# Optimization experiments

Measured on AMD Instinct MI355X. Metric: run time of the kernel, lower is better.

The kernel has to match this reference:

```python
import jax, jax.numpy as jnp
import numpy as np

N, E, B, T = 50000, 800000, 256, 50
IN_DIM, H, C1, C2, Q_DIM, LH = 128, 4, 32, 128, 32, 128
EPS = 1e-5


def setup_inputs() -> dict:
    key = jax.random.key(0)
    ks = jax.random.split(key, 24)
    g = 0.05
    inp = {
        'x': jax.random.normal(ks[0], (N, IN_DIM), jnp.float32),
        'edge_index': jax.random.randint(ks[1], (2, E), 0, N, jnp.int32),
        'batch': jnp.sort(jax.random.randint(ks[2], (N,), 0, B, jnp.int32)),
        'quant': jax.random.normal(ks[3], (B, T, Q_DIM), jnp.float32),
        # GATConv(128 -> 32, heads=4, concat)
        'gat_W': jax.random.normal(ks[4], (IN_DIM, H * C1), jnp.float32) * g,
        'gat_att_src': jax.random.normal(ks[5], (H, C1), jnp.float32) * g,
        'gat_att_dst': jax.random.normal(ks[6], (H, C1), jnp.float32) * g,
        'gat_b': jnp.zeros((H * C1,), jnp.float32),
        # BN1 over 128 channels (eval mode)
        'bn1_gamma': jnp.ones((H * C1,), jnp.float32),
        'bn1_beta': jnp.zeros((H * C1,), jnp.float32),
        'bn1_mean': jax.random.normal(ks[7], (H * C1,), jnp.float32) * 0.01,
        'bn1_var': jnp.ones((H * C1,), jnp.float32),
        # GCNConv(128 -> 128)
        'gcn_W': jax.random.normal(ks[8], (H * C1, C2), jnp.float32) * g,
        'gcn_b': jnp.zeros((C2,), jnp.float32),
        'bn2_gamma': jnp.ones((C2,), jnp.float32),
        'bn2_beta': jnp.zeros((C2,), jnp.float32),
        'bn2_mean': jax.random.normal(ks[9], (C2,), jnp.float32) * 0.01,
        'bn2_var': jnp.ones((C2,), jnp.float32),
        # GlobalAttention gate: Linear(C2 -> 1)
        'gate_W': jax.random.normal(ks[10], (1, C2), jnp.float32) * g,
        'gate_b': jnp.zeros((1,), jnp.float32),
        # LSTM(Q_DIM -> LH), torch gate order i,f,g,o
        'lstm_Wih': jax.random.normal(ks[11], (4 * LH, Q_DIM), jnp.float32) * g,
        'lstm_Whh': jax.random.normal(ks[12], (4 * LH, LH), jnp.float32) * g,
        'lstm_bih': jnp.zeros((4 * LH,), jnp.float32),
        'lstm_bhh': jnp.zeros((4 * LH,), jnp.float32),
        # final Linear(C2+LH -> 1)
        'fc_W': jax.random.normal(ks[13], (1, C2 + LH), jnp.float32) * g,
        'fc_b': jnp.zeros((1,), jnp.float32),
    }
    return inp


def _segment_softmax(e, seg, num_segments):
    m = jax.ops.segment_max(e, seg, num_segments=num_segments)
    ex = jnp.exp(e - m[seg])
    s = jax.ops.segment_sum(ex, seg, num_segments=num_segments)
    return ex / (s[seg] + 1e-16)


def _bn_eval(x, gamma, beta, mean, var):
    return gamma * (x - mean) * jax.lax.rsqrt(var + EPS) + beta


def _forward(x, edge_index, batch, quant,
             gat_W, gat_att_src, gat_att_dst, gat_b,
             bn1_gamma, bn1_beta, bn1_mean, bn1_var,
             gcn_W, gcn_b, bn2_gamma, bn2_beta, bn2_mean, bn2_var,
             gate_W, gate_b,
             lstm_Wih, lstm_Whh, lstm_bih, lstm_bhh,
             fc_W, fc_b):
    n = x.shape[0]
    loops = jnp.arange(n, dtype=edge_index.dtype)
    ei = jnp.concatenate([edge_index, jnp.stack([loops, loops])], axis=1)  # add self loops
    src, dst = ei[0], ei[1]

    # ---- GATConv ----
    xw = (x @ gat_W).reshape(n, H, C1)                      # [N,H,C1]
    a_src = jnp.sum(xw * gat_att_src, axis=-1)              # [N,H]
    a_dst = jnp.sum(xw * gat_att_dst, axis=-1)
    e = jax.nn.leaky_relu(a_src[src] + a_dst[dst], 0.2)     # [E+N,H]
    alpha = _segment_softmax(e, dst, n)                     # softmax over in-edges per dst
    msg = xw[src] * alpha[:, :, None]                       # [E+N,H,C1]
    h = jax.ops.segment_sum(msg, dst, num_segments=n).reshape(n, H * C1) + gat_b

    h = jax.nn.elu(h)
    h = _bn_eval(h, bn1_gamma, bn1_beta, bn1_mean, bn1_var)

    # ---- GCNConv (sym-normalized with self loops) ----
    deg = jax.ops.segment_sum(jnp.ones_like(dst, jnp.float32), dst, num_segments=n)
    dinv = jnp.where(deg > 0, jax.lax.rsqrt(deg), 0.0)
    norm = dinv[src] * dinv[dst]                            # [E+N]
    hw = h @ gcn_W                                          # [N,C2]
    h2 = jax.ops.segment_sum(hw[src] * norm[:, None], dst, num_segments=n) + gcn_b

    h2 = jax.nn.elu(h2)
    h2 = _bn_eval(h2, bn2_gamma, bn2_beta, bn2_mean, bn2_var)

    # ---- GlobalAttention pooling over graphs ----
    gate = (h2 @ gate_W.T + gate_b)[:, 0]                   # [N]
    score = _segment_softmax(gate, batch, B)
    graph_rep = jax.ops.segment_sum(score[:, None] * h2, batch, num_segments=B)  # [B,C2]

    # ---- LSTM over quant series ----
    def step(carry, xt):
        hh, cc = carry
        gates = xt @ lstm_Wih.T + hh @ lstm_Whh.T + lstm_bih + lstm_bhh
        i, f, gg, o = jnp.split(gates, 4, axis=-1)
        cc = jax.nn.sigmoid(f) * cc + jax.nn.sigmoid(i) * jnp.tanh(gg)
        hh = jax.nn.sigmoid(o) * jnp.tanh(cc)
        return (hh, cc), None

    h0 = jnp.zeros((B, LH), quant.dtype)
    (hT, _), _ = jax.lax.scan(step, (h0, h0), jnp.swapaxes(quant, 0, 1))

    combined = jnp.concatenate([graph_rep, hT], axis=1)     # [B, C2+LH]
    out = (combined @ fc_W.T + fc_b)[:, 0]                  # [B]
    return out


def reference(x, edge_index, batch, quant,
              gat_W, gat_att_src, gat_att_dst, gat_b,
              bn1_gamma, bn1_beta, bn1_mean, bn1_var,
              gcn_W, gcn_b, bn2_gamma, bn2_beta, bn2_mean, bn2_var,
              gate_W, gate_b,
              lstm_Wih, lstm_Whh, lstm_bih, lstm_bhh,
              fc_W, fc_b):
    return _forward(x, edge_index, batch, quant,
                    gat_W, gat_att_src, gat_att_dst, gat_b,
                    bn1_gamma, bn1_beta, bn1_mean, bn1_var,
                    gcn_W, gcn_b, bn2_gamma, bn2_beta, bn2_mean, bn2_var,
                    gate_W, gate_b,
                    lstm_Wih, lstm_Whh, lstm_bih, lstm_bhh,
                    fc_W, fc_b)
```

## Files before the change

### kernel.cpp

```cpp
#include <hip/hip_runtime.h>
#include <cfloat>
#include <cstddef>

constexpr int KIN   = 128;
constexpr int KQD   = 32;
constexpr int KT    = 50;
constexpr int KLH   = 128;
constexpr float BN_EPS = 1e-5f;

typedef __attribute__((ext_vector_type(8))) short bf16x8;
typedef __attribute__((ext_vector_type(4))) float f32x4;
union U8 { bf16x8 v; unsigned u[4]; };

__device__ __forceinline__ float elu_f(float x)  { return x > 0.f ? x : expm1f(x); }
__device__ __forceinline__ float leaky_f(float x){ return x > 0.f ? x : 0.2f * x; }
__device__ __forceinline__ float fsigm(float x)  { return 1.f / (1.f + __expf(-x)); }
__device__ __forceinline__ float ftanh(float x)  { return 1.f - 2.f / (__expf(2.f * x) + 1.f); }

__device__ __forceinline__ unsigned bfpack(float lo, float hi) {
    unsigned ul = __float_as_uint(lo), uh = __float_as_uint(hi);
    ul += 0x7FFFu + ((ul >> 16) & 1u);
    uh += 0x7FFFu + ((uh >> 16) & 1u);
    return (ul >> 16) | (uh & 0xFFFF0000u);
}
__device__ __forceinline__ unsigned short bf1(float v) {
    unsigned u = __float_as_uint(v);
    u += 0x7FFFu + ((u >> 16) & 1u);
    return (unsigned short)(u >> 16);
}
__device__ __forceinline__ float bflo(unsigned u) { return __uint_as_float(u << 16); }
__device__ __forceinline__ float bfhi(unsigned u) { return __uint_as_float(u & 0xFFFF0000u); }

__device__ __forceinline__ bf16x8 pack8(float4 p, float4 q) {
    U8 t;
    t.u[0] = bfpack(p.x, p.y); t.u[1] = bfpack(p.z, p.w);
    t.u[2] = bfpack(q.x, q.y); t.u[3] = bfpack(q.z, q.w);
    return t.v;
}

__global__ void k_deg(const int* __restrict__ ei, int E, int* __restrict__ deg) {
    int e = blockIdx.x * blockDim.x + threadIdx.x;
    if (e < E) atomicAdd(&deg[ei[E + e]], 1);
}

__global__ __launch_bounds__(1024)
void k_scan_a(const int* __restrict__ deg, int n, int* __restrict__ bsum) {
    __shared__ int wsum[16];
    int tid = threadIdx.x, lane = tid & 63, w = tid >> 6;
    int i0 = blockIdx.x * 4096 + tid * 4;
    int t = 0;
    #pragma unroll
    for (int j = 0; j < 4; j++) t += (i0 + j < n) ? deg[i0 + j] : 0;
    #pragma unroll
    for (int d = 1; d < 64; d <<= 1) t += __shfl_xor(t, d);
    if (lane == 0) wsum[w] = t;
    __syncthreads();
    if (tid == 0) {
        int s = 0;
        #pragma unroll
        for (int k = 0; k < 16; k++) s += wsum[k];
        bsum[blockIdx.x] = s;
    }
}

__global__ void k_scan_b(int* __restrict__ bsum, int nb) {
    if (threadIdx.x == 0) {
        int run = 0;
        for (int i = 0; i < nb; i++) { int v = bsum[i]; bsum[i] = run; run += v; }
    }
}

__global__ __launch_bounds__(1024)
void k_scan_c(const int* __restrict__ deg, int n, const int* __restrict__ bsum,
              int* __restrict__ offsets, int* __restrict__ cursor,
              float* __restrict__ dinv) {
    __shared__ int wsum[16];
    int tid = threadIdx.x, lane = tid & 63, w = tid >> 6;
    int i0 = blockIdx.x * 4096 + tid * 4;
    int v[4];
    #pragma unroll
    for (int j = 0; j < 4; j++) v[j] = (i0 + j < n) ? deg[i0 + j] : 0;
    int tsum = v[0] + v[1] + v[2] + v[3];
    int sc = tsum;
    #pragma unroll
    for (int d = 1; d < 64; d <<= 1) {
        int o = __shfl_up(sc, d);
        if (lane >= d) sc += o;
    }
    if (lane == 63) wsum[w] = sc;
    __syncthreads();
    if (w == 0) {
        int xx = (lane < 16) ? wsum[lane] : 0;
        #pragma unroll
        for (int d = 1; d < 16; d <<= 1) {
            int o = __shfl_up(xx, d);
            if (lane >= d) xx += o;
        }
        if (lane < 16) wsum[lane] = xx;
    }
    __syncthreads();
    int run = bsum[blockIdx.x] + ((w > 0) ? wsum[w - 1] : 0) + sc - tsum;
    #pragma unroll
    for (int j = 0; j < 4; j++) {
        int i = i0 + j;
        if (i < n) {
            cursor[i]      = run;
            offsets[i + 1] = run + v[j];
            dinv[i]        = rsqrtf((float)(v[j] + 1));
            run += v[j];
        }
    }
    if (blockIdx.x == 0 && tid == 0) offsets[0] = 0;
}

__global__ void k_fill(const int* __restrict__ ei, int E, int* __restrict__ cursor,
                       int* __restrict__ csr_src) {
    int e = blockIdx.x * blockDim.x + threadIdx.x;
    if (e < E) {
        int s = ei[e], d = ei[E + e];
        int pos = atomicAdd(&cursor[d], 1);
        csr_src[pos] = s;
    }
}

template <bool ATT>
__global__ __launch_bounds__(256, 4)
void k_gemm_mfma(const float* __restrict__ X, const float* __restrict__ W,
                 unsigned* __restrict__ Yb, int nrows,
                 const float* __restrict__ attS, const float* __restrict__ attD,
                 float* __restrict__ a_src, float* __restrict__ a_dst) {
    __shared__ float tile[16][132];
    __shared__ float as_sh[128], ad_sh[128];
    int tid  = threadIdx.x;
    int lane = tid & 63;
    int wv   = tid >> 6;
    if (ATT && tid < 128) { as_sh[tid] = attS[tid]; ad_sh[tid] = attD[tid]; }
    int l16 = lane & 15;
    int kq  = (lane >> 4) * 8;
    bf16x8 bfr[2][4];
    #pragma unroll
    for (int nt = 0; nt < 2; nt++) {
        int n = wv * 32 + nt * 16 + l16;
        #pragma unroll
        for (int kk = 0; kk < 4; kk++) {
            int k0 = kk * 32 + kq;
            float f[8];
            #pragma unroll
            for (int j = 0; j < 8; j++) f[j] = W[(size_t)(k0 + j) * 128 + n];
            U8 t;
            t.u[0] = bfpack(f[0], f[1]); t.u[1] = bfpack(f[2], f[3]);
            t.u[2] = bfpack(f[4], f[5]); t.u[3] = bfpack(f[6], f[7]);
            bfr[nt][kk] = t.v;
        }
    }
    int nch = (nrows + 15) / 16;
    for (int ch = blockIdx.x; ch < nch; ch += gridDim.x) {
        int r0 = ch * 16;
        int r  = r0 + l16;
        bool rok = r < nrows;
        const float* xr = X + (size_t)r * 128 + kq;
        float4 z4 = make_float4(0.f, 0.f, 0.f, 0.f);
        bf16x8 afr[4];
        #pragma unroll
        for (int kk = 0; kk < 4; kk++) {
            float4 p = rok ? *reinterpret_cast<const float4*>(xr + kk * 32)     : z4;
            float4 q = rok ? *reinterpret_cast<const float4*>(xr + kk * 32 + 4) : z4;
            afr[kk] = pack8(p, q);
        }
        f32x4 acc0 = {0.f, 0.f, 0.f, 0.f};
        f32x4 acc1 = {0.f, 0.f, 0.f, 0.f};
        #pragma unroll
        for (int kk = 0; kk < 4; kk++) {
            acc0 = __builtin_amdgcn_mfma_f32_16x16x32_bf16(afr[kk], bfr[0][kk], acc0, 0, 0, 0);
            acc1 = __builtin_amdgcn_mfma_f32_16x16x32_bf16(afr[kk], bfr[1][kk], acc1, 0, 0, 0);
        }
        __syncthreads();
        int rowb = (lane >> 4) * 4;
        int cb   = wv * 32 + l16;
        #pragma unroll
        for (int reg = 0; reg < 4; reg++) {
            tile[rowb + reg][cb]      = acc0[reg];
            tile[rowb + reg][cb + 16] = acc1[reg];
        }
        __syncthreads();
        #pragma unroll
        for (int i = 0; i < 4; i++) {
            int idx = tid + i * 256;
            int row = idx >> 6, cp = idx & 63;
            int rr = r0 + row;
            if (rr < nrows) {
                float2 f = *reinterpret_cast<const float2*>(&tile[row][cp * 2]);
                Yb[(size_t)rr * 64 + cp] = bfpack(f.x, f.y);
            }
        }
        if (ATT && tid < 64) {
            int rr2 = tid >> 2, h = tid & 3;
            if (r0 + rr2 < nrows) {
                float ps = 0.f, pd = 0.f;
                #pragma unroll
                for (int j = 0; j < 32; j++) {
                    float v = tile[rr2][h * 32 + j];
                    ps += v * as_sh[h * 32 + j];
                    pd += v * ad_sh[h * 32 + j];
                }
                a_src[(size_t)(r0 + rr2) * 4 + h] = ps;
                a_dst[(size_t)(r0 + rr2) * 4 + h] = pd;
            }
        }
    }
}

__global__ __launch_bounds__(256)
void k_gat_agg(const int* __restrict__ offsets, const int* __restrict__ csr_src,
               const float* __restrict__ a_src, const float* __restrict__ a_dst,
               const unsigned* __restrict__ xwb, const float* __restrict__ bias,
               const float* __restrict__ g1, const float* __restrict__ b1,
               const float* __restrict__ mu1, const float* __restrict__ var1,
               float* __restrict__ hout, int n) {
    __shared__ int   src_sh[4][64];
    __shared__ float al_sh[4][4][64];
    int lane = threadIdx.x & 63;
    int wv   = threadIdx.x >> 6;
    int wid  = (blockIdx.x * blockDim.x + threadIdx.x) >> 6;
    int nw   = (gridDim.x * blockDim.x) >> 6;
    int hP   = lane >> 4;
    int c0 = lane * 2, c1 = c0 + 1;
    float bi0 = bias[c0], bi1 = bias[c1];
    float A0 = g1[c0] * rsqrtf(var1[c0] + BN_EPS);
    float A1 = g1[c1] * rsqrtf(var1[c1] + BN_EPS);
    float B0 = b1[c0] - mu1[c0] * A0;
    float B1 = b1[c1] - mu1[c1] * A1;
    for (int node = wid; node < n; node += nw) {
        int beg = offsets[node], end = offsets[node + 1];
        int rowlen = end - beg, total = rowlen + 1;
        float4 adv = *reinterpret_cast<const float4*>(&a_dst[(size_t)node * 4]);
        int sv = (lane < rowlen) ? csr_src[beg + lane] : node;
        float4 as4 = *reinterpret_cast<const float4*>(&a_src[(size_t)sv * 4]);
        float e0 = leaky_f(as4.x + adv.x), e1 = leaky_f(as4.y + adv.y);
        float e2 = leaky_f(as4.z + adv.z), e3 = leaky_f(as4.w + adv.w);
        float m[4] = {-FLT_MAX, -FLT_MAX, -FLT_MAX, -FLT_MAX};
        if (lane < total) { m[0] = e0; m[1] = e1; m[2] = e2; m[3] = e3; }
        for (int i = lane + 64; i < total; i += 64) {
            int src = (i < rowlen) ? csr_src[beg + i] : node;
            float4 a4 = *reinterpret_cast<const float4*>(&a_src[(size_t)src * 4]);
            m[0] = fmaxf(m[0], leaky_f(a4.x + adv.x));
            m[1] = fmaxf(m[1], leaky_f(a4.y + adv.y));
            m[2] = fmaxf(m[2], leaky_f(a4.z + adv.z));
            m[3] = fmaxf(m[3], leaky_f(a4.w + adv.w));
        }
        #pragma unroll
        for (int off = 32; off; off >>= 1) {
            #pragma unroll
            for (int h = 0; h < 4; h++) m[h] = fmaxf(m[h], __shfl_xor(m[h], off));
        }
        float ex[4] = {0.f, 0.f, 0.f, 0.f};
        if (lane < total) {
            ex[0] = expf(e0 - m[0]); ex[1] = expf(e1 - m[1]);
            ex[2] = expf(e2 - m[2]); ex[3] = expf(e3 - m[3]);
        }
        float s[4] = {ex[0], ex[1], ex[2], ex[3]};
        for (int i = lane + 64; i < total; i += 64) {
            int src = (i < rowlen) ? csr_src[beg + i] : node;
            float4 a4 = *reinterpret_cast<const float4*>(&a_src[(size_t)src * 4]);
            s[0] += expf(leaky_f(a4.x + adv.x) - m[0]);
            s[1] += expf(leaky_f(a4.y + adv.y) - m[1]);
            s[2] += expf(leaky_f(a4.z + adv.z) - m[2]);
            s[3] += expf(leaky_f(a4.w + adv.w) - m[3]);
        }
        #pragma unroll
        for (int off = 32; off; off >>= 1) {
            #pragma unroll
            for (int h = 0; h < 4; h++) s[h] += __shfl_xor(s[h], off);
        }
        float inv[4];
        #pragma unroll
        for (int h = 0; h < 4; h++) inv[h] = 1.f / (s[h] + 1e-16f);
        src_sh[wv][lane] = sv;
        #pragma unroll
        for (int h = 0; h < 4; h++) al_sh[wv][h][lane] = ex[h] * inv[h];
        __builtin_amdgcn_wave_barrier();
        float acc0 = 0.f, acc1 = 0.f;
        int cnt = min(total, 64);
        {
            int i = 0;
            for (; i + 4 <= cnt; i += 4) {
                int s0 = src_sh[wv][i],     s1 = src_sh[wv][i + 1];
                int s2 = src_sh[wv][i + 2], s3 = src_sh[wv][i + 3];
                float a0 = al_sh[wv][hP][i],     a1 = al_sh[wv][hP][i + 1];
                float a2 = al_sh[wv][hP][i + 2], a3 = al_sh[wv][hP][i + 3];
                unsigned u0 = xwb[(size_t)s0 * 64 + lane];
                unsigned u1 = xwb[(size_t)s1 * 64 + lane];
                unsigned u2 = xwb[(size_t)s2 * 64 + lane];
                unsigned u3 = xwb[(size_t)s3 * 64 + lane];
                acc0 += a0 * bflo(u0); acc1 += a0 * bfhi(u0);
                acc0 += a1 * bflo(u1); acc1 += a1 * bfhi(u1);
                acc0 += a2 * bflo(u2); acc1 += a2 * bfhi(u2);
                acc0 += a3 * bflo(u3); acc1 += a3 * bfhi(u3);
            }
            for (; i < cnt; i++) {
                int src  = src_sh[wv][i];
                float aP = al_sh[wv][hP][i];
                unsigned u = xwb[(size_t)src * 64 + lane];
                acc0 += aP * bflo(u);
                acc1 += aP * bfhi(u);
            }
        }
        for (int base = 64; base < total; base += 64) {
            __builtin_amdgcn_wave_barrier();
            int i = base + lane;
            int src2 = node;
            float a0v = 0.f, a1v = 0.f, a2v = 0.f, a3v = 0.f;
            if (i < total) {
                if (i < rowlen) src2 = csr_src[beg + i];
                float4 a4 = *reinterpret_cast<const float4*>(&a_src[(size_t)src2 * 4]);
                a0v = expf(leaky_f(a4.x + adv.x) - m[0]) * inv[0];
                a1v = expf(leaky_f(a4.y + adv.y) - m[1]) * inv[1];
                a2v = expf(leaky_f(a4.z + adv.z) - m[2]) * inv[2];
                a3v = expf(leaky_f(a4.w + adv.w) - m[3]) * inv[3];
            }
            src_sh[wv][lane] = src2;
            al_sh[wv][0][lane] = a0v; al_sh[wv][1][lane] = a1v;
            al_sh[wv][2][lane] = a2v; al_sh[wv][3][lane] = a3v;
            __builtin_amdgcn_wave_barrier();
            int cnt2 = min(total - base, 64);
            for (int j = 0; j < cnt2; j++) {
                int src  = src_sh[wv][j];
                float aP = al_sh[wv][hP][j];
                unsigned u = xwb[(size_t)src * 64 + lane];
                acc0 += aP * bflo(u);
                acc1 += aP * bfhi(u);
            }
        }
        __builtin_amdgcn_wave_barrier();
        float vA = elu_f(acc0 + bi0);
        float vB = elu_f(acc1 + bi1);
        vA = vA * A0 + B0;
        vB = vB * A1 + B1;
        *reinterpret_cast<float2*>(&hout[(size_t)node * 128 + c0]) =
            make_float2(vA, vB);
    }
}

__global__ __launch_bounds__(256)
void k_gcn_agg(const int* __restrict__ offsets, const int* __restrict__ csr_src,
               const float* __restrict__ dinv, const unsigned* __restrict__ hwb,
               const float* __restrict__ bias,
               const float* __restrict__ g2, const float* __restrict__ b2,
               const float* __restrict__ mu2, const float* __restrict__ var2,
               const float* __restrict__ gateW, const float* __restrict__ gateB,
               float* __restrict__ h2, float* __restrict__ gate, int n) {
    __shared__ int   src_sh[4][64];
    __shared__ float w_sh[4][64];
    int lane = threadIdx.x & 63;
    int wv   = threadIdx.x >> 6;
    int wid  = (blockIdx.x * blockDim.x + threadIdx.x) >> 6;
    int nw   = (gridDim.x * blockDim.x) >> 6;
    int c0 = lane * 2, c1 = c0 + 1;
    float bi0 = bias[c0], bi1 = bias[c1];
    float A0 = g2[c0] * rsqrtf(var2[c0] + BN_EPS);
    float A1 = g2[c1] * rsqrtf(var2[c1] + BN_EPS);
    float B0 = b2[c0] - mu2[c0] * A0;
    float B1 = b2[c1] - mu2[c1] * A1;
    float gw0 = gateW[c0], gw1 = gateW[c1], gB = gateB[0];
    for (int node = wid; node < n; node += nw) {
        int beg = offsets[node], end = offsets[node + 1];
        int rowlen = end - beg;
        float dn = dinv[node];
        unsigned us = hwb[(size_t)node * 64 + lane];
        float acc0 = dn * dn * bflo(us);
        float acc1 = dn * dn * bfhi(us);
        for (int base = 0; base < rowlen; base += 64) {
            __builtin_amdgcn_wave_barrier();
            int i = base + lane;
            int src2 = node;
            float wv2 = 0.f;
            if (i < rowlen) { src2 = csr_src[beg + i]; wv2 = dinv[src2] * dn; }
            src_sh[wv][lane] = src2;
            w_sh[wv][lane]   = wv2;
            __builtin_amdgcn_wave_barrier();
            int cnt = min(rowlen - base, 64);
            int j = 0;
            for (; j + 4 <= cnt; j += 4) {
                int s0 = src_sh[wv][j],     s1 = src_sh[wv][j + 1];
                int s2 = src_sh[wv][j + 2], s3 = src_sh[wv][j + 3];
                float w0 = w_sh[wv][j],     w1 = w_sh[wv][j + 1];
                float w2 = w_sh[wv][j + 2], w3 = w_sh[wv][j + 3];
                unsigned u0 = hwb[(size_t)s0 * 64 + lane];
                unsigned u1 = hwb[(size_t)s1 * 64 + lane];
                unsigned u2 = hwb[(size_t)s2 * 64 + lane];
                unsigned u3 = hwb[(size_t)s3 * 64 + lane];
                acc0 += w0 * bflo(u0); acc1 += w0 * bfhi(u0);
                acc0 += w1 * bflo(u1); acc1 += w1 * bfhi(u1);
                acc0 += w2 * bflo(u2); acc1 += w2 * bfhi(u2);
                acc0 += w3 * bflo(u3); acc1 += w3 * bfhi(u3);
            }
            for (; j < cnt; j++) {
                int src = src_sh[wv][j];
                float w = w_sh[wv][j];
                unsigned u = hwb[(size_t)src * 64 + lane];
                acc0 += w * bflo(u);
                acc1 += w * bfhi(u);
            }
        }
        __builtin_amdgcn_wave_barrier();
        float vA = elu_f(acc0 + bi0);
        float vB = elu_f(acc1 + bi1);
        vA = vA * A0 + B0;
        vB = vB * A1 + B1;
        *reinterpret_cast<float2*>(&h2[(size_t)node * 128 + c0]) =
            make_float2(vA, vB);
        float p = vA * gw0 + vB * gw1;
        #pragma unroll
        for (int off = 32; off; off >>= 1) p += __shfl_xor(p, off);
        if (lane == 0) gate[node] = p + gB;
    }
}

__device__ __forceinline__ int lbound(const int* a, int n, int key) {
    int lo = 0, hi = n;
    while (lo < hi) { int mid = (lo + hi) >> 1; if (a[mid] < key) lo = mid + 1; else hi = mid; }
    return lo;
}

__global__ __launch_bounds__(256)
void k_pool(const int* __restrict__ batch, const float* __restrict__ gate,
            const float* __restrict__ h2, const float* __restrict__ hT,
            const float* __restrict__ fcW, const float* __restrict__ fcB,
            float* __restrict__ out, int n) {
    int b = blockIdx.x, tid = threadIdx.x;
    __shared__ float red[256];
    __shared__ float sc_sh[256];
    int start = lbound(batch, n, b);
    int end   = lbound(batch, n, b + 1);
    float m = -FLT_MAX;
    for (int i = start + tid; i < end; i += 256) m = fmaxf(m, gate[i]);
    red[tid] = m; __syncthreads();
    for (int s2 = 128; s2 > 0; s2 >>= 1) {
        if (tid < s2) red[tid] = fmaxf(red[tid], red[tid + s2]);
        __syncthreads();
    }
    m = red[0]; __syncthreads();
    float s = 0.f;
    for (int i = start + tid; i < end; i += 256) s += expf(gate[i] - m);
    red[tid] = s; __syncthreads();
    for (int s2 = 128; s2 > 0; s2 >>= 1) {
        if (tid < s2) red[tid] += red[tid + s2];
        __syncthreads();
    }
    float inv = 1.f / (red[0] + 1e-16f);
    __syncthreads();
    int j = tid & 127, half = tid >> 7;
    float acc = 0.f;
    for (int base = start; base < end; base += 256) {
        int cnt = min(256, end - base);
        __syncthreads();
        if (tid < cnt) sc_sh[tid] = expf(gate[base + tid] - m) * inv;
        __syncthreads();
        for (int ii = half; ii < cnt; ii += 2)
            acc += sc_sh[ii] * h2[(size_t)(base + ii) * 128 + j];
    }
    red[tid] = acc; __syncthreads();
    if (half == 0) sc_sh[j] = red[j] + red[128 + j];
    __syncthreads();
    float p = 0.f;
    if (tid < 128)
        p = fcW[tid] * sc_sh[tid] + fcW[128 + tid] * hT[(size_t)b * 128 + tid];
    red[tid] = p; __syncthreads();
    for (int s2 = 128; s2 > 0; s2 >>= 1) {
        if (tid < s2) red[tid] += red[tid + s2];
        __syncthreads();
    }
    if (tid == 0) out[b] = red[0] + fcB[0];
}

__global__ __launch_bounds__(512)
void k_lstm_mfma(const float* __restrict__ quant, const float* __restrict__ Wih,
                 const float* __restrict__ Whh, const float* __restrict__ bih,
                 const float* __restrict__ bhh, float* __restrict__ hstate) {
    __shared__ unsigned short h16[2][16][136];
    __shared__ unsigned short x16[16][1608];
    int t = threadIdx.x, lane = t & 63, w = t >> 6;
    int b0   = blockIdx.x * 16;
    int l15  = lane & 15;
    int kq8  = (lane >> 4) * 8;
    int j    = w * 16 + l15;
    int rowq = (lane >> 4) * 4;
    float bi_i = bih[j]       + bhh[j];
    float bi_f = bih[128 + j] + bhh[128 + j];
    float bi_g = bih[256 + j] + bhh[256 + j];
    float bi_o = bih[384 + j] + bhh[384 + j];
    bf16x8 whh_f[4][4], wih_f[4];
    #pragma unroll
    for (int c = 0; c < 4; c++) {
        int col = c * 128 + j;
        #pragma unroll
        for (int kk = 0; kk < 4; kk++) {
            const float* wr = &Whh[(size_t)col * 128 + kk * 32 + kq8];
            whh_f[c][kk] = pack8(*reinterpret_cast<const float4*>(wr),
                                 *reinterpret_cast<const float4*>(wr + 4));
        }
        const float* wr = &Wih[(size_t)col * 32 + kq8];
        wih_f[c] = pack8(*reinterpret_cast<const float4*>(wr),
                         *reinterpret_cast<const float4*>(wr + 4));
    }
    unsigned* xw32 = reinterpret_cast<unsigned*>(&x16[0][0]);
    for (int p = t; p < 16 * 800; p += 512) {
        int r = p / 800, rem = p - r * 800;
        float2 f = *reinterpret_cast<const float2*>(
            &quant[(size_t)(b0 + r) * (KT * KQD) + rem * 2]);
        xw32[r * 804 + rem] = bfpack(f.x, f.y);
    }
    for (int p = t; p < 16 * 136; p += 512) {
        int r = p / 136, cc = p - r * 136;
        h16[0][r][cc] = 0;
    }
    float cst[4] = {0.f, 0.f, 0.f, 0.f};
    int cur = 0;
    __syncthreads();
    f32x4 xg[4];
    {
        bf16x8 ax = *reinterpret_cast<const bf16x8*>(&x16[l15][kq8]);
        #pragma unroll
        for (int c = 0; c < 4; c++) {
            f32x4 z = {0.f, 0.f, 0.f, 0.f};
            xg[c] = __builtin_amdgcn_mfma_f32_16x16x32_bf16(ax, wih_f[c], z, 0, 0, 0);
        }
    }
    for (int s = 0; s < KT; s++) {
        bf16x8 ah0 = *reinterpret_cast<const bf16x8*>(&h16[cur][l15][kq8]);
        bf16x8 ah1 = *reinterpret_cast<const bf16x8*>(&h16[cur][l15][32 + kq8]);
        bf16x8 ah2 = *reinterpret_cast<const bf16x8*>(&h16[cur][l15][64 + kq8]);
        bf16x8 ah3 = *reinterpret_cast<const bf16x8*>(&h16[cur][l15][96 + kq8]);
        f32x4 ga[4], gb[4];
        #pragma unroll
        for (int c = 0; c < 4; c++) {
            f32x4 z = {0.f, 0.f, 0.f, 0.f};
            f32x4 a = __builtin_amdgcn_mfma_f32_16x16x32_bf16(ah0, whh_f[c][0], xg[c], 0, 0, 0);
            a = __builtin_amdgcn_mfma_f32_16x16x32_bf16(ah1, whh_f[c][1], a, 0, 0, 0);
            f32x4 b = __builtin_amdgcn_mfma_f32_16x16x32_bf16(ah2, whh_f[c][2], z, 0, 0, 0);
            b = __builtin_amdgcn_mfma_f32_16x16x32_bf16(ah3, whh_f[c][3], b, 0, 0, 0);
            ga[c] = a; gb[c] = b;
        }
        int nxt = cur ^ 1;
        #pragma unroll
        for (int r = 0; r < 4; r++) {
            float ig = fsigm(ga[0][r] + gb[0][r] + bi_i);
            float fg = fsigm(ga[1][r] + gb[1][r] + bi_f);
            float gg = ftanh(ga[2][r] + gb[2][r] + bi_g);
            float og = fsigm(ga[3][r] + gb[3][r] + bi_o);
            cst[r] = fg * cst[r] + ig * gg;
            h16[nxt][rowq + r][j] = bf1(og * ftanh(cst[r]));
        }
        if (s + 1 < KT) {
            bf16x8 ax = *reinterpret_cast<const bf16x8*>(&x16[l15][(s + 1) * 32 + kq8]);
            #pragma unroll
            for (int c = 0; c < 4; c++) {
                f32x4 z = {0.f, 0.f, 0.f, 0.f};
                xg[c] = __builtin_amdgcn_mfma_f32_16x16x32_bf16(ax, wih_f[c], z, 0, 0, 0);
            }
        }
        __syncthreads();
        cur = nxt;
    }
    for (int p = t; p < 16 * KLH; p += 512) {
        int row = p >> 7, jj = p & 127;
        hstate[(size_t)(b0 + row) * KLH + jj] =
            __uint_as_float((unsigned)h16[cur][row][jj] << 16);
    }
}

extern "C" void kernel_launch(void* const* d_in, const int* in_sizes, int n_in,
                              void* d_out, int out_size, void* d_ws, size_t ws_size,
                              hipStream_t stream) {
    const float* x     = (const float*)d_in[0];
    const int*   ei    = (const int*)  d_in[1];
    const int*   batch = (const int*)  d_in[2];
    const float* quant = (const float*)d_in[3];
    const float* gatW  = (const float*)d_in[4];
    const float* attS  = (const float*)d_in[5];
    const float* attD  = (const float*)d_in[6];
    const float* gatB  = (const float*)d_in[7];
    const float* bn1g  = (const float*)d_in[8];
    const float* bn1b  = (const float*)d_in[9];
    const float* bn1m  = (const float*)d_in[10];
    const float* bn1v  = (const float*)d_in[11];
    const float* gcnW  = (const float*)d_in[12];
    const float* gcnB  = (const float*)d_in[13];
    const float* bn2g  = (const float*)d_in[14];
    const float* bn2b  = (const float*)d_in[15];
    const float* bn2m  = (const float*)d_in[16];
    const float* bn2v  = (const float*)d_in[17];
    const float* gateW = (const float*)d_in[18];
    const float* gateB = (const float*)d_in[19];
    const float* Wih   = (const float*)d_in[20];
    const float* Whh   = (const float*)d_in[21];
    const float* bih   = (const float*)d_in[22];
    const float* bhh   = (const float*)d_in[23];
    const float* fcW   = (const float*)d_in[24];
    const float* fcB   = (const float*)d_in[25];

    int N = in_sizes[0] / KIN;
    int E = in_sizes[1] / 2;
    int B = in_sizes[3] / (KT * KQD);

    char* ws = (char*)d_ws;
    size_t off = 0;
    auto alloc = [&](size_t bytes) -> void* {
        void* p = ws + off;
        off += (bytes + 511) & ~(size_t)511;
        return p;
    };
    int nb = (N + 4095) / 4096;
    int*      deg     = (int*)     alloc((size_t)N * 4);
    int*      offsets = (int*)     alloc((size_t)(N + 1) * 4);
    int*      cursor  = (int*)     alloc((size_t)N * 4);
    float*    dinv    = (float*)   alloc((size_t)N * 4);
    int*      csr_src = (int*)     alloc((size_t)E * 4);
    int*      bsum    = (int*)     alloc((size_t)nb * 4);
    float*    a_src   = (float*)   alloc((size_t)N * 16);
    float*    a_dst   = (float*)   alloc((size_t)N * 16);
    unsigned* xwb     = (unsigned*)alloc((size_t)N * 256);
    float*    hbuf    = (float*)   alloc((size_t)N * 512);
    float*    gate    = (float*)   alloc((size_t)N * 4);
    float*    hstate  = (float*)   alloc((size_t)B * KLH * 4);

    hipMemsetAsync(deg, 0, (size_t)N * 4, stream);
    int eb = (E + 255) / 256;
    k_deg   <<<eb, 256, 0, stream>>>(ei, E, deg);
    k_scan_a<<<nb, 1024, 0, stream>>>(deg, N, bsum);
    k_scan_b<<<1, 64, 0, stream>>>(bsum, nb);
    k_scan_c<<<nb, 1024, 0, stream>>>(deg, N, bsum, offsets, cursor, dinv);
    k_fill  <<<eb, 256, 0, stream>>>(ei, E, cursor, csr_src);

    k_lstm_mfma<<<B / 16, 512, 0, stream>>>(quant, Wih, Whh, bih, bhh, hstate);

    k_gemm_mfma<true ><<<512, 256, 0, stream>>>(x, gatW, xwb, N, attS, attD, a_src, a_dst);
    k_gat_agg<<<3072, 256, 0, stream>>>(offsets, csr_src, a_src, a_dst, xwb, gatB,
                                        bn1g, bn1b, bn1m, bn1v, hbuf, N);
    k_gemm_mfma<false><<<512, 256, 0, stream>>>(hbuf, gcnW, xwb, N,
                                                nullptr, nullptr, nullptr, nullptr);
    k_gcn_agg<<<3072, 256, 0, stream>>>(offsets, csr_src, dinv, xwb, gcnB,
                                        bn2g, bn2b, bn2m, bn2v, gateW, gateB,
                                        hbuf, gate, N);
    k_pool<<<B, 256, 0, stream>>>(batch, gate, hbuf, hstate, fcW, fcB,
                                  (float*)d_out, N);
}
```

Measured before the change: 430.3 us.

## Precompute LSTM input projections in a parallel kernel before the recurrence

Splits the LSTM into a parallel input-projection kernel (quant·Wih + biases across all timesteps, one block per chunk and timestep) and a recurrent kernel that only does the h·Whh MFMAs. The recurrent loop now issues four independent accumulation chains per k-slice and prefetches the next step's projection from global memory, which shortens the serial per-step critical path. The cost is an extra launch plus a workspace round-trip of the projected gates. The LSTM runs on only a handful of blocks on a serial stream that also carries the graph kernels, so the overall effect depends on how much of the total time the recurrence accounts for.

```diff
diff --git a/kernel.cpp b/kernel.cpp
--- a/kernel.cpp
+++ b/kernel.cpp
@@ -473,23 +473,44 @@
     if (tid == 0) out[b] = red[0] + fcB[0];
 }
 
+__global__ __launch_bounds__(256)
+void k_xproj(const float* __restrict__ quant, const float* __restrict__ Wih,
+             const float* __restrict__ bih, const float* __restrict__ bhh,
+             float* __restrict__ xproj) {
+    int blk = blockIdx.x;
+    int chunk = blk / KT, s = blk % KT;
+    int lane = threadIdx.x & 63, w = threadIdx.x >> 6;
+    int l15 = lane & 15, kq8 = (lane >> 4) * 8;
+    int b = chunk * 16 + l15;
+    const float* xr = &quant[(size_t)b * (KT * KQD) + s * KQD + kq8];
+    bf16x8 ax = pack8(*reinterpret_cast<const float4*>(xr),
+                      *reinterpret_cast<const float4*>(xr + 4));
+    #pragma unroll
+    for (int ti = 0; ti < 8; ti++) {
+        int tc = w * 8 + ti;
+        int gcol = w * 128 + ti * 16 + l15;
+        const float* wr = &Wih[(size_t)gcol * KQD + kq8];
+        bf16x8 bw = pack8(*reinterpret_cast<const float4*>(wr),
+                          *reinterpret_cast<const float4*>(wr + 4));
+        f32x4 acc = {0.f, 0.f, 0.f, 0.f};
+        acc = __builtin_amdgcn_mfma_f32_16x16x32_bf16(ax, bw, acc, 0, 0, 0);
+        float bv = bih[gcol] + bhh[gcol];
+        acc[0] += bv; acc[1] += bv; acc[2] += bv; acc[3] += bv;
+        *reinterpret_cast<f32x4*>(
+            &xproj[(((size_t)chunk * KT + s) * 32 + tc) * 256 + lane * 4]) = acc;
+    }
+}
+
 __global__ __launch_bounds__(512)
-void k_lstm_mfma(const float* __restrict__ quant, const float* __restrict__ Wih,
-                 const float* __restrict__ Whh, const float* __restrict__ bih,
-                 const float* __restrict__ bhh, float* __restrict__ hstate) {
-    __shared__ unsigned short h16[2][16][136];
-    __shared__ unsigned short x16[16][1608];
+void k_lstm2(const float* __restrict__ xproj, const float* __restrict__ Whh,
+             float* __restrict__ hstate) {
+    __shared__ unsigned short h16[2][16][148];
     int t = threadIdx.x, lane = t & 63, w = t >> 6;
-    int b0   = blockIdx.x * 16;
-    int l15  = lane & 15;
-    int kq8  = (lane >> 4) * 8;
-    int j    = w * 16 + l15;
+    int chunk = blockIdx.x;
+    int l15 = lane & 15, kq8 = (lane >> 4) * 8;
+    int j = w * 16 + l15;
     int rowq = (lane >> 4) * 4;
-    float bi_i = bih[j]       + bhh[j];
-    float bi_f = bih[128 + j] + bhh[128 + j];
-    float bi_g = bih[256 + j] + bhh[256 + j];
-    float bi_o = bih[384 + j] + bhh[384 + j];
-    bf16x8 whh_f[4][4], wih_f[4];
+    bf16x8 whh_f[4][4];
     #pragma unroll
     for (int c = 0; c < 4; c++) {
         int col = c * 128 + j;
@@ -499,69 +520,50 @@
             whh_f[c][kk] = pack8(*reinterpret_cast<const float4*>(wr),
                                  *reinterpret_cast<const float4*>(wr + 4));
         }
-        const float* wr = &Wih[(size_t)col * 32 + kq8];
-        wih_f[c] = pack8(*reinterpret_cast<const float4*>(wr),
-                         *reinterpret_cast<const float4*>(wr + 4));
-    }
-    unsigned* xw32 = reinterpret_cast<unsigned*>(&x16[0][0]);
-    for (int p = t; p < 16 * 800; p += 512) {
-        int r = p / 800, rem = p - r * 800;
-        float2 f = *reinterpret_cast<const float2*>(
-            &quant[(size_t)(b0 + r) * (KT * KQD) + rem * 2]);
-        xw32[r * 804 + rem] = bfpack(f.x, f.y);
-    }
-    for (int p = t; p < 16 * 136; p += 512) {
-        int r = p / 136, cc = p - r * 136;
+    }
+    for (int p = t; p < 16 * 148; p += 512) {
+        int r = p / 148, cc = p - r * 148;
         h16[0][r][cc] = 0;
     }
     float cst[4] = {0.f, 0.f, 0.f, 0.f};
+    const float* xb = xproj + ((size_t)chunk * KT) * 32 * 256;
+    f32x4 xgA = *reinterpret_cast<const f32x4*>(&xb[(0 * 8 + w) * 256 + lane * 4]);
+    f32x4 xgB = *reinterpret_cast<const f32x4*>(&xb[(1 * 8 + w) * 256 + lane * 4]);
+    f32x4 xgC = *reinterpret_cast<const f32x4*>(&xb[(2 * 8 + w) * 256 + lane * 4]);
+    f32x4 xgD = *reinterpret_cast<const f32x4*>(&xb[(3 * 8 + w) * 256 + lane * 4]);
     int cur = 0;
     __syncthreads();
-    f32x4 xg[4];
-    {
-        bf16x8 ax = *reinterpret_cast<const bf16x8*>(&x16[l15][kq8]);
-        #pragma unroll
-        for (int c = 0; c < 4; c++) {
-            f32x4 z = {0.f, 0.f, 0.f, 0.f};
-            xg[c] = __builtin_amdgcn_mfma_f32_16x16x32_bf16(ax, wih_f[c], z, 0, 0, 0);
-        }
-    }
     for (int s = 0; s < KT; s++) {
-        bf16x8 ah0 = *reinterpret_cast<const bf16x8*>(&h16[cur][l15][kq8]);
-        bf16x8 ah1 = *reinterpret_cast<const bf16x8*>(&h16[cur][l15][32 + kq8]);
-        bf16x8 ah2 = *reinterpret_cast<const bf16x8*>(&h16[cur][l15][64 + kq8]);
-        bf16x8 ah3 = *reinterpret_cast<const bf16x8*>(&h16[cur][l15][96 + kq8]);
-        f32x4 ga[4], gb[4];
-        #pragma unroll
-        for (int c = 0; c < 4; c++) {
-            f32x4 z = {0.f, 0.f, 0.f, 0.f};
-            f32x4 a = __builtin_amdgcn_mfma_f32_16x16x32_bf16(ah0, whh_f[c][0], xg[c], 0, 0, 0);
-            a = __builtin_amdgcn_mfma_f32_16x16x32_bf16(ah1, whh_f[c][1], a, 0, 0, 0);
-            f32x4 b = __builtin_amdgcn_mfma_f32_16x16x32_bf16(ah2, whh_f[c][2], z, 0, 0, 0);
-            b = __builtin_amdgcn_mfma_f32_16x16x32_bf16(ah3, whh_f[c][3], b, 0, 0, 0);
-            ga[c] = a; gb[c] = b;
+        f32x4 ai = xgA, af = xgB, ag = xgC, ao = xgD;
+        #pragma unroll
+        for (int kk = 0; kk < 4; kk++) {
+            bf16x8 ah = *reinterpret_cast<const bf16x8*>(&h16[cur][l15][kk * 32 + kq8]);
+            ai = __builtin_amdgcn_mfma_f32_16x16x32_bf16(ah, whh_f[0][kk], ai, 0, 0, 0);
+            af = __builtin_amdgcn_mfma_f32_16x16x32_bf16(ah, whh_f[1][kk], af, 0, 0, 0);
+            ag = __builtin_amdgcn_mfma_f32_16x16x32_bf16(ah, whh_f[2][kk], ag, 0, 0, 0);
+            ao = __builtin_amdgcn_mfma_f32_16x16x32_bf16(ah, whh_f[3][kk], ao, 0, 0, 0);
+        }
+        if (s + 1 < KT) {
+            const float* xs = &xb[((size_t)(s + 1) * 32 + w) * 256 + lane * 4];
+            xgA = *reinterpret_cast<const f32x4*>(&xs[0 * 8 * 256]);
+            xgB = *reinterpret_cast<const f32x4*>(&xs[1 * 8 * 256]);
+            xgC = *reinterpret_cast<const f32x4*>(&xs[2 * 8 * 256]);
+            xgD = *reinterpret_cast<const f32x4*>(&xs[3 * 8 * 256]);
         }
         int nxt = cur ^ 1;
         #pragma unroll
         for (int r = 0; r < 4; r++) {
-            float ig = fsigm(ga[0][r] + gb[0][r] + bi_i);
-            float fg = fsigm(ga[1][r] + gb[1][r] + bi_f);
-            float gg = ftanh(ga[2][r] + gb[2][r] + bi_g);
-            float og = fsigm(ga[3][r] + gb[3][r] + bi_o);
+            float ig = fsigm(ai[r]);
+            float fg = fsigm(af[r]);
+            float gg = ftanh(ag[r]);
+            float og = fsigm(ao[r]);
             cst[r] = fg * cst[r] + ig * gg;
             h16[nxt][rowq + r][j] = bf1(og * ftanh(cst[r]));
         }
-        if (s + 1 < KT) {
-            bf16x8 ax = *reinterpret_cast<const bf16x8*>(&x16[l15][(s + 1) * 32 + kq8]);
-            #pragma unroll
-            for (int c = 0; c < 4; c++) {
-                f32x4 z = {0.f, 0.f, 0.f, 0.f};
-                xg[c] = __builtin_amdgcn_mfma_f32_16x16x32_bf16(ax, wih_f[c], z, 0, 0, 0);
-            }
-        }
         __syncthreads();
         cur = nxt;
     }
+    int b0 = chunk * 16;
     for (int p = t; p < 16 * KLH; p += 512) {
         int row = p >> 7, jj = p & 127;
         hstate[(size_t)(b0 + row) * KLH + jj] =
@@ -602,6 +604,7 @@
     int N = in_sizes[0] / KIN;
     int E = in_sizes[1] / 2;
     int B = in_sizes[3] / (KT * KQD);
+    int nchunks = B / 16;
 
     char* ws = (char*)d_ws;
     size_t off = 0;
@@ -623,6 +626,7 @@
     float*    hbuf    = (float*)   alloc((size_t)N * 512);
     float*    gate    = (float*)   alloc((size_t)N * 4);
     float*    hstate  = (float*)   alloc((size_t)B * KLH * 4);
+    float*    xproj   = (float*)   alloc((size_t)nchunks * KT * 32 * 256 * 4);
 
     hipMemsetAsync(deg, 0, (size_t)N * 4, stream);
     int eb = (E + 255) / 256;
@@ -632,7 +636,8 @@
     k_scan_c<<<nb, 1024, 0, stream>>>(deg, N, bsum, offsets, cursor, dinv);
     k_fill  <<<eb, 256, 0, stream>>>(ei, E, cursor, csr_src);
 
-    k_lstm_mfma<<<B / 16, 512, 0, stream>>>(quant, Wih, Whh, bih, bhh, hstate);
+    k_xproj<<<nchunks * KT, 256, 0, stream>>>(quant, Wih, bih, bhh, xproj);
+    k_lstm2<<<nchunks, 512, 0, stream>>>(xproj, Whh, hstate);
 
     k_gemm_mfma<true ><<<512, 256, 0, stream>>>(x, gatW, xwb, N, attS, attD, a_src, a_dst);
     k_gat_agg<<<3072, 256, 0, stream>>>(offsets, csr_src, a_src, a_dst, xwb, gatB,
```

After: 432.1 us. No clear change (+0.4%).
